# Optimization experiments

Measured on AMD Instinct MI355X. Metric: run time of the kernel, lower is better.

## Reference

```python
import jax, jax.numpy as jnp
import numpy as np

B, S, H = 2, 4096, 1024
NH, BS, NR = 16, 64, 3
HD = H // NH
NB = S // BS
PEN = -10000.0


def setup_inputs():
    key = jax.random.key(0)
    k0, k1, k2, k3 = jax.random.split(key, 4)
    s = 0.02
    inp = {
        'hidden_states': jax.random.normal(k0, (B, S, H), jnp.float32),
        'attention_mask': jnp.ones((B, S), jnp.float32),
        'Wq': jax.random.normal(k1, (H, H), jnp.float32) * s,
        'Wk': jax.random.normal(k2, (H, H), jnp.float32) * s,
        'Wv': jax.random.normal(k3, (H, H), jnp.float32) * s,
        'bq': jnp.zeros((H,), jnp.float32),
        'bk': jnp.zeros((H,), jnp.float32),
        'bv': jnp.zeros((H,), jnp.float32),
    }
    rng = np.random.default_rng(0)
    inp['rand_attn'] = jnp.asarray(rng.integers(1, NB - 1, size=(B, NH, NB - 2, NR)), jnp.int32)
    return inp


def _attend(q_blk, kmat, vmat, mask, rsd):
    # q_blk:[b,h,q,d]  kmat/vmat:[b,h,k,d]  mask: multiplicative {0,1} broadcastable to [b,h,q,k]
    p = jnp.einsum('bhqd,bhkd->bhqk', q_blk, kmat) * rsd + (1.0 - mask) * PEN
    return jnp.einsum('bhqk,bhkd->bhqd', jax.nn.softmax(p, axis=-1), vmat)


def reference(hidden_states, attention_mask, Wq, bq, Wk, bk, Wv, bv, rand_attn):
    b, s, _ = hidden_states.shape
    h, d, bs = NH, HD, BS
    nb = s // bs
    rsd = 1.0 / jnp.sqrt(jnp.asarray(d, hidden_states.dtype))

    def proj(W, bias):
        return (hidden_states @ W + bias).reshape(b, s, h, d).transpose(0, 2, 1, 3)

    q, k, v = proj(Wq, bq), proj(Wk, bk), proj(Wv, bv)  # [b,h,s,d]

    # --- masks (create_masks_for_block_sparse_attn)
    bm = attention_mask.reshape(b, nb, bs)
    band_mask = jnp.einsum('blq,blk->blqk', bm[:, 2:-2],
                           jnp.concatenate([bm[:, 1:-3], bm[:, 2:-2], bm[:, 3:-1]], axis=2))[:, None]
    from_mask = attention_mask.reshape(b, 1, s, 1)
    to_mask = attention_mask.reshape(b, 1, 1, s)

    qb = q.reshape(b, h, nb, bs, d)
    kb = k.reshape(b, h, nb, bs, d)
    vb = v.reshape(b, h, nb, bs, d)

    # --- gather random blocks (jax_gather with batch_dims=2)
    gather2 = jax.vmap(jax.vmap(lambda m, i: m[i]))
    gk = gather2(kb, rand_attn).reshape(b, h, nb - 2, NR * bs, d)
    gv = gather2(vb, rand_attn).reshape(b, h, nb - 2, NR * bs, d)
    rm = jax.vmap(lambda m, i: m[i])(bm, rand_attn).reshape(b, h, nb - 2, NR * bs)
    rand_mask = jnp.einsum('blq,bhlk->bhlqk', bm[:, 1:-1], rm)  # [b,h,nb-2,bs,NR*bs]

    # --- block 0: attends to everything
    first_ctx = _attend(qb[:, :, 0], k, v, to_mask, rsd)[:, :, None]

    # --- block 1: first 3 blocks + last block + its random blocks
    ones_r = jnp.ones((b, 1, 1, NR * bs), q.dtype)
    sk = jnp.concatenate([kb[:, :, 0], kb[:, :, 1], kb[:, :, 2], kb[:, :, -1], gk[:, :, 0]], axis=2)
    sv = jnp.concatenate([vb[:, :, 0], vb[:, :, 1], vb[:, :, 2], vb[:, :, -1], gv[:, :, 0]], axis=2)
    seq_pad = jnp.concatenate([to_mask[:, :, :, :3 * bs], to_mask[:, :, :, -bs:], ones_r], axis=3)
    rand_pad = jnp.concatenate([jnp.ones((b, h, bs, 4 * bs), q.dtype), rand_mask[:, :, 0]], axis=3)
    second_ctx = _attend(qb[:, :, 1], sk, sv, jnp.minimum(seq_pad, rand_pad), rsd)[:, :, None]

    # --- middle blocks 2..nb-3: sliding band + random + first-global + last-global
    mq = qb[:, :, 2:-2]  # [b,h,L,bs,d], L = nb-4
    ek = jnp.concatenate([kb[:, :, 1:-3], kb[:, :, 2:-2], kb[:, :, 3:-1]], axis=3)  # [b,h,L,3bs,d]
    ev = jnp.concatenate([vb[:, :, 1:-3], vb[:, :, 2:-2], vb[:, :, 3:-1]], axis=3)
    band_p = jnp.einsum('bhlqd,bhlkd->bhlqk', mq, ek) * rsd + (1.0 - band_mask) * PEN
    rand_p = jnp.einsum('bhlqd,bhlkd->bhlqk', mq, gk[:, :, 1:-1]) * rsd + (1.0 - rand_mask[:, :, 1:-1]) * PEN
    first_p = jnp.einsum('bhlqd,bhkd->bhlqk', mq, kb[:, :, 0]) * rsd \
        + (1.0 - to_mask[:, :, :, :bs][:, :, :, None]) * PEN
    last_p = jnp.einsum('bhlqd,bhkd->bhlqk', mq, kb[:, :, -1]) * rsd \
        + (1.0 - to_mask[:, :, :, -bs:][:, :, :, None]) * PEN
    # scores layout: [first(bs) | band(3bs) | rand(NR*bs) | last(bs)]
    w = jax.nn.softmax(jnp.concatenate([first_p, band_p, rand_p, last_p], axis=-1), axis=-1)
    mid_ctx = jnp.einsum('bhlqk,bhlkd->bhlqd', w[..., bs:4 * bs], ev)
    mid_ctx += jnp.einsum('bhlqk,bhlkd->bhlqd', w[..., 4 * bs:-bs], gv[:, :, 1:-1])
    mid_ctx += jnp.einsum('bhlqk,bhkd->bhlqd', w[..., :bs], vb[:, :, 0])
    mid_ctx += jnp.einsum('bhlqk,bhkd->bhlqd', w[..., -bs:], vb[:, :, -1])

    # --- block nb-2: first block + last 3 blocks + its random blocks
    slk = jnp.concatenate([kb[:, :, 0], kb[:, :, -3], kb[:, :, -2], kb[:, :, -1], gk[:, :, -1]], axis=2)
    slv = jnp.concatenate([vb[:, :, 0], vb[:, :, -3], vb[:, :, -2], vb[:, :, -1], gv[:, :, -1]], axis=2)
    seq_pad = jnp.concatenate([to_mask[:, :, :, :bs], to_mask[:, :, :, -3 * bs:], ones_r], axis=3)
    rand_pad = jnp.concatenate([jnp.ones((b, h, bs, 4 * bs), q.dtype), rand_mask[:, :, -1]], axis=3)
    seclast_ctx = _attend(qb[:, :, -2], slk, slv, jnp.minimum(seq_pad, rand_pad), rsd)[:, :, None]

    # --- last block: attends to everything
    last_ctx = _attend(qb[:, :, -1], k, v, to_mask, rsd)[:, :, None]

    ctx = jnp.concatenate([first_ctx, second_ctx, mid_ctx, seclast_ctx, last_ctx], axis=2)
    ctx = ctx.reshape(b, h, s, d) * from_mask
    return ctx.transpose(0, 2, 1, 3).reshape(b, s, h * d)
```

## Files before the change

kernel.cpp:

```cpp
#include <hip/hip_runtime.h>

typedef unsigned short u16;
typedef short short8 __attribute__((ext_vector_type(8)));
typedef float f32x4 __attribute__((ext_vector_type(4)));

#define S_TOT 4096
#define NHEAD 16
#define HD 64
#define NB 64
#define BS 64
#define M0 16.0f

__device__ __forceinline__ u16 f2bf(float f) {
    unsigned int u = __builtin_bit_cast(unsigned int, f);
    unsigned int r = (u + 0x7fffu + ((u >> 16) & 1u)) >> 16;
    return (u16)r;
}

__device__ __forceinline__ void gload_lds16(const void* g, void* l) {
    __builtin_amdgcn_global_load_lds(
        (const __attribute__((address_space(1))) unsigned int*)g,
        (__attribute__((address_space(3))) unsigned int*)l, 16, 0, 0);
}

__device__ __forceinline__ float rsum16(float v) {
    v += __shfl_xor(v, 1);
    v += __shfl_xor(v, 2);
    v += __shfl_xor(v, 4);
    v += __shfl_xor(v, 8);
    return v;
}

__global__ __launch_bounds__(256) void convH(const float* __restrict__ h, u16* __restrict__ A) {
    size_t i = (size_t)blockIdx.x * blockDim.x + threadIdx.x;
    float4 v = ((const float4*)h)[i];
    ushort4 o;
    o.x = f2bf(v.x); o.y = f2bf(v.y); o.z = f2bf(v.z); o.w = f2bf(v.w);
    ((ushort4*)A)[i] = o;
}

__global__ __launch_bounds__(256) void transW(const float* __restrict__ Wq,
                                              const float* __restrict__ Wk,
                                              const float* __restrict__ Wv,
                                              u16* __restrict__ Wt) {
    const float* W = blockIdx.z == 0 ? Wq : (blockIdx.z == 1 ? Wk : Wv);
    u16* T = Wt + (size_t)blockIdx.z * 1024 * 1024;
    __shared__ float tile[64][65];
    int n0 = blockIdx.x * 64, k0 = blockIdx.y * 64;
    int tx = threadIdx.x, ty = threadIdx.y;
    for (int r = ty; r < 64; r += 4) tile[r][tx] = W[(size_t)(k0 + r) * 1024 + n0 + tx];
    __syncthreads();
    for (int r = ty; r < 64; r += 4) T[(size_t)(n0 + r) * 1024 + k0 + tx] = f2bf(tile[tx][r]);
}

__global__ __launch_bounds__(256) void gemmQKV(const u16* __restrict__ Ah, const u16* __restrict__ Wt,
                                               const float* __restrict__ bq, const float* __restrict__ bk,
                                               const float* __restrict__ bv,
                                               u16* __restrict__ Qb, u16* __restrict__ Kb,
                                               u16* __restrict__ Vtb) {
    int mode = blockIdx.z;
    const u16* W = Wt + (size_t)mode * 1024 * 1024;
    const float* bias = mode == 0 ? bq : (mode == 1 ? bk : bv);
    __shared__ alignas(16) u16 As[128 * 64];
    __shared__ alignas(16) u16 Bs[128 * 64];
    int tid = threadIdx.x;
    int wave = tid >> 6, lane = tid & 63;
    int lo = lane & 15, hi = lane >> 4;
    int m0 = blockIdx.x * 128, n0 = blockIdx.y * 128;
    int wr = wave >> 1, wc = wave & 1;
    f32x4 acc[4][4];
#pragma unroll
    for (int i = 0; i < 4; i++)
#pragma unroll
        for (int j = 0; j < 4; j++) acc[i][j] = f32x4{0.f, 0.f, 0.f, 0.f};

    for (int k0 = 0; k0 < 1024; k0 += 64) {
#pragma unroll
        for (int i = 0; i < 4; i++) {
            int c = i * 256 + tid;
            int row = c >> 3, c8 = c & 7;
            gload_lds16(Ah + (size_t)(m0 + row) * 1024 + k0 + c8 * 8, As + (i * 256 + wave * 64) * 8);
            gload_lds16(W + (size_t)(n0 + row) * 1024 + k0 + c8 * 8, Bs + (i * 256 + wave * 64) * 8);
        }
        __syncthreads();
#pragma unroll
        for (int kk = 0; kk < 2; kk++) {
            short8 a[4], bb[4];
#pragma unroll
            for (int mi = 0; mi < 4; mi++)
                a[mi] = *(const short8*)&As[(wr * 64 + mi * 16 + lo) * 64 + kk * 32 + hi * 8];
#pragma unroll
            for (int ni = 0; ni < 4; ni++)
                bb[ni] = *(const short8*)&Bs[(wc * 64 + ni * 16 + lo) * 64 + kk * 32 + hi * 8];
#pragma unroll
            for (int mi = 0; mi < 4; mi++)
#pragma unroll
                for (int ni = 0; ni < 4; ni++)
                    acc[mi][ni] = __builtin_amdgcn_mfma_f32_16x16x32_bf16(a[mi], bb[ni], acc[mi][ni], 0, 0, 0);
        }
        __syncthreads();
    }
#pragma unroll
    for (int ni = 0; ni < 4; ni++) {
        int n = n0 + wc * 64 + ni * 16 + lo;
        float bv_ = bias[n];
        int hh = n >> 6, d = n & 63;
        if (mode < 2) {
            u16* T = (mode == 0) ? Qb : Kb;
#pragma unroll
            for (int mi = 0; mi < 4; mi++) {
                int mb = m0 + wr * 64 + mi * 16 + hi * 4;
                int b_ = mb >> 12, s = mb & 4095;
                size_t base = (((size_t)b_ * NHEAD + hh) * S_TOT + s) * HD + d;
#pragma unroll
                for (int r = 0; r < 4; r++) T[base + (size_t)r * HD] = f2bf(acc[mi][ni][r] + bv_);
            }
        } else {
#pragma unroll
            for (int mi = 0; mi < 4; mi++) {
                int mb = m0 + wr * 64 + mi * 16 + hi * 4;
                int b_ = mb >> 12, s = mb & 4095;
                ushort4 pk;
                pk.x = f2bf(acc[mi][ni][0] + bv_);
                pk.y = f2bf(acc[mi][ni][1] + bv_);
                pk.z = f2bf(acc[mi][ni][2] + bv_);
                pk.w = f2bf(acc[mi][ni][3] + bv_);
                *(ushort4*)&Vtb[(((size_t)b_ * NHEAD + hh) * HD + d) * S_TOT + s] = pk;
            }
        }
    }
}

__global__ __launch_bounds__(256) void bigbird_attn(const u16* __restrict__ Qb, const u16* __restrict__ Kb,
                                                    const u16* __restrict__ Vtb, const float* __restrict__ am,
                                                    const int* __restrict__ rand_attn, float* __restrict__ out,
                                                    float* __restrict__ po, float* __restrict__ pl) {
    int lx = blockIdx.x;
    int h = blockIdx.y, b = blockIdx.z;
    bool heavy = lx < 16;
    int p = lx & 7;
    int l = heavy ? ((lx >> 3) ? 63 : 0) : (lx - 15);
    int bh = b * NHEAD + h;
    const u16* Qh = Qb + (size_t)bh * S_TOT * HD;
    const u16* Kh = Kb + (size_t)bh * S_TOT * HD;
    const u16* Vh = Vtb + (size_t)bh * HD * S_TOT;
    int tid = threadIdx.x, wave = tid >> 6, lane = tid & 63;
    int lo = lane & 15, hi = lane >> 4;

    __shared__ int klist[64];
    __shared__ int knum_s;
    __shared__ alignas(16) u16 Kls[2][64 * 64];
    __shared__ alignas(16) u16 Vls[2][64 * 64];
    __shared__ alignas(16) u16 Plds[4][16 * 64];

    auto STAGE = [&](int buf, int kblk) {
        const char* Kc = (const char*)(Kh + (size_t)kblk * BS * HD);
        const char* Vc = (const char*)(Vh + kblk * BS);
#pragma unroll
        for (int i = 0; i < 2; i++) {
            int off = i * 4096 + wave * 1024 + lane * 16;
            int row = off >> 7, c = off & 127;
            int cs = c ^ ((row & 7) << 4);
            gload_lds16(Kc + row * 128 + cs, (char*)Kls[buf] + i * 4096 + wave * 1024);
            gload_lds16(Vc + row * 8192 + cs, (char*)Vls[buf] + i * 4096 + wave * 1024);
        }
    };

    if (tid == 0) {
        if (heavy) {
            for (int i = 0; i < 8; i++) klist[i] = p * 8 + i;
            knum_s = 8;
        } else {
            int q = 0;
            klist[q++] = 0;
            if (l == 1) { klist[q++] = 1; klist[q++] = 2; }
            else if (l == 62) { klist[q++] = 61; klist[q++] = 62; }
            else { klist[q++] = l - 1; klist[q++] = l; klist[q++] = l + 1; }
            klist[q++] = 63;
            const int* ra = rand_attn + (((size_t)b * NHEAD + h) * 62 + (l - 1)) * 3;
            klist[q++] = ra[0]; klist[q++] = ra[1]; klist[q++] = ra[2];
            knum_s = q;
        }
    }
    STAGE(0, heavy ? p * 8 : 0);
    __syncthreads();

    int kn = knum_s;
    int qrow = l * BS + wave * 16;

    short8 qf[2];
#pragma unroll
    for (int kk = 0; kk < 2; kk++)
        qf[kk] = *(const short8*)&Qh[(size_t)(qrow + lo) * HD + kk * 32 + hi * 8];

    float ls[4];
    f32x4 oacc[4];
#pragma unroll
    for (int r = 0; r < 4; r++) ls[r] = 0.f;
#pragma unroll
    for (int n = 0; n < 4; n++) oacc[n] = f32x4{0.f, 0.f, 0.f, 0.f};
    char* pbase = (char*)&Plds[wave][0];

    int buf = 0;
    for (int ci = 0; ci < kn; ci++) {
        int kbase = klist[ci] * BS;
        if (ci + 1 < kn) STAGE(buf ^ 1, klist[ci + 1]);
        float pen[4];
#pragma unroll
        for (int t = 0; t < 4; t++) pen[t] = (1.0f - am[b * S_TOT + kbase + t * 16 + lo]) * (-10000.0f) - M0;
        f32x4 sc[4];
#pragma unroll
        for (int t = 0; t < 4; t++) {
            f32x4 c = f32x4{0.f, 0.f, 0.f, 0.f};
#pragma unroll
            for (int kk = 0; kk < 2; kk++) {
                int kr = t * 16 + lo;
                int a = (kr * 128 + kk * 64 + hi * 16) ^ ((kr & 7) << 4);
                short8 kf = *(const short8*)((char*)Kls[buf] + a);
                c = __builtin_amdgcn_mfma_f32_16x16x32_bf16(qf[kk], kf, c, 0, 0, 0);
            }
            sc[t] = c;
        }
#pragma unroll
        for (int t = 0; t < 4; t++)
#pragma unroll
            for (int r = 0; r < 4; r++) {
                float pr = __expf(sc[t][r] * 0.125f + pen[t]);
                ls[r] += pr;
                int row = hi * 4 + r, col = t * 16 + lo;
                int off = (row * 128 + col * 2) ^ ((row & 7) << 4);
                *(u16*)(pbase + off) = f2bf(pr);
            }
#pragma unroll
        for (int kk = 0; kk < 2; kk++) {
            int off = (lo * 128 + kk * 64 + hi * 16) ^ ((lo & 7) << 4);
            short8 pf = *(const short8*)(pbase + off);
#pragma unroll
            for (int n = 0; n < 4; n++) {
                int vr = n * 16 + lo;
                int a = (vr * 128 + kk * 64 + hi * 16) ^ ((vr & 7) << 4);
                short8 vf = *(const short8*)((char*)Vls[buf] + a);
                oacc[n] = __builtin_amdgcn_mfma_f32_16x16x32_bf16(pf, vf, oacc[n], 0, 0, 0);
            }
        }
        __syncthreads();
        buf ^= 1;
    }

    if (heavy) {
        int combo = (bh << 1) | (l ? 1 : 0);
        int base = (combo * 8 + p) * 64;
#pragma unroll
        for (int r = 0; r < 4; r++) {
            int qr = wave * 16 + hi * 4 + r;
            float lsum = rsum16(ls[r]);
            if (lo == 0) pl[base + qr] = lsum;
#pragma unroll
            for (int n = 0; n < 4; n++)
                po[(size_t)(base + qr) * 64 + n * 16 + lo] = oacc[n][r];
        }
    } else {
#pragma unroll
        for (int r = 0; r < 4; r++) {
            float lsum = rsum16(ls[r]);
            int q = qrow + hi * 4 + r;
            float qm = am[b * S_TOT + q];
            float iv = qm / lsum;
#pragma unroll
            for (int n = 0; n < 4; n++)
                out[((size_t)b * S_TOT + q) * 1024 + h * HD + n * 16 + lo] = oacc[n][r] * iv;
        }
    }
}

__global__ __launch_bounds__(256) void reduce_heavy(const float* __restrict__ po, const float* __restrict__ pl,
                                                    const float* __restrict__ am, float* __restrict__ out) {
    int combo = blockIdx.x;
    int b = combo >> 5, h = (combo >> 1) & 15, hv = combo & 1;
    int l = hv ? 63 : 0;
    for (int idx = threadIdx.x; idx < 4096; idx += 256) {
        int qr = idx >> 6, d = idx & 63;
        float s = 0.f, lsum = 0.f;
#pragma unroll
        for (int p = 0; p < 8; p++) {
            s += po[(size_t)((combo * 8 + p) * 64 + qr) * 64 + d];
            lsum += pl[(combo * 8 + p) * 64 + qr];
        }
        int q = l * BS + qr;
        float qm = am[b * S_TOT + q];
        out[((size_t)b * S_TOT + q) * 1024 + h * HD + d] = s / lsum * qm;
    }
}

extern "C" void kernel_launch(void* const* d_in, const int* in_sizes, int n_in,
                              void* d_out, int out_size, void* d_ws, size_t ws_size,
                              hipStream_t stream) {
    const float* hidden = (const float*)d_in[0];
    const float* am = (const float*)d_in[1];
    const float* Wq = (const float*)d_in[2];
    const float* Wk = (const float*)d_in[3];
    const float* Wv = (const float*)d_in[4];
    const float* bq = (const float*)d_in[5];
    const float* bk = (const float*)d_in[6];
    const float* bv = (const float*)d_in[7];
    const int* rand_attn = (const int*)d_in[8];
    float* out = (float*)d_out;

    char* w = (char*)d_ws;
    u16* Ah = (u16*)w;  w += (size_t)8192 * 1024 * 2;
    u16* Wt = (u16*)w;  w += (size_t)3 * 1024 * 1024 * 2;
    u16* Qb = (u16*)w;  w += (size_t)2 * 16 * 4096 * 64 * 2;
    u16* Kb = (u16*)w;  w += (size_t)2 * 16 * 4096 * 64 * 2;
    u16* Vtb = (u16*)w;
    float* po = (float*)Ah;
    float* pl = po + (size_t)64 * 8 * 64 * 64;

    convH<<<8192, 256, 0, stream>>>(hidden, Ah);
    transW<<<dim3(16, 16, 3), dim3(64, 4), 0, stream>>>(Wq, Wk, Wv, Wt);
    gemmQKV<<<dim3(64, 8, 3), 256, 0, stream>>>(Ah, Wt, bq, bk, bv, Qb, Kb, Vtb);
    bigbird_attn<<<dim3(78, 16, 2), 256, 0, stream>>>(Qb, Kb, Vtb, am, rand_attn, out, po, pl);
    reduce_heavy<<<64, 256, 0, stream>>>(po, pl, am, out);
}
```

Baseline: 165.5 us.

## Double-buffer QKV GEMM with swizzled LDS, block remap, and LDS-staged epilogue

```diff
diff --git a/kernel.cpp b/kernel.cpp
--- a/kernel.cpp
+++ b/kernel.cpp
@@ -53,80 +53,134 @@
     for (int r = ty; r < 64; r += 4) T[(size_t)(n0 + r) * 1024 + k0 + tx] = f2bf(tile[tx][r]);
 }
 
-__global__ __launch_bounds__(256) void gemmQKV(const u16* __restrict__ Ah, const u16* __restrict__ Wt,
-                                               const float* __restrict__ bq, const float* __restrict__ bk,
-                                               const float* __restrict__ bv,
-                                               u16* __restrict__ Qb, u16* __restrict__ Kb,
-                                               u16* __restrict__ Vtb) {
-    int mode = blockIdx.z;
-    const u16* W = Wt + (size_t)mode * 1024 * 1024;
+__global__ __launch_bounds__(256, 2) void gemm_fused(const u16* __restrict__ Ah, const u16* __restrict__ Wt,
+                                                     const float* __restrict__ bq, const float* __restrict__ bk,
+                                                     const float* __restrict__ bv,
+                                                     u16* __restrict__ Qb, u16* __restrict__ Kb,
+                                                     u16* __restrict__ Vtb) {
+    __shared__ alignas(16) char lds[2][32768];
+
+    int bid = blockIdx.x;
+    int swz = (bid & 7) * 192 + (bid >> 3);
+    int bm = swz & 63, bn = swz >> 6;
+    int m0 = bm * 128, n0 = bn * 128;
+    int mode = bn >> 3;
     const float* bias = mode == 0 ? bq : (mode == 1 ? bk : bv);
-    __shared__ alignas(16) u16 As[128 * 64];
-    __shared__ alignas(16) u16 Bs[128 * 64];
-    int tid = threadIdx.x;
-    int wave = tid >> 6, lane = tid & 63;
+    int tid = threadIdx.x, wave = tid >> 6, lane = tid & 63;
     int lo = lane & 15, hi = lane >> 4;
-    int m0 = blockIdx.x * 128, n0 = blockIdx.y * 128;
     int wr = wave >> 1, wc = wave & 1;
+
+    const char* Ac = (const char*)Ah;
+    const char* Wc = (const char*)Wt;
+
+    auto STAGE = [&](int buf, int t) {
+#pragma unroll
+        for (int i = 0; i < 4; i++) {
+            int off = i * 4096 + tid * 16;
+            int row = off >> 7, cb = off & 127;
+            int cs = cb ^ ((row & 7) << 4);
+            char* d = lds[buf] + i * 4096 + wave * 1024;
+            gload_lds16(Ac + (size_t)(m0 + row) * 2048 + t * 128 + cs, d);
+            gload_lds16(Wc + (size_t)(n0 + row) * 2048 + t * 128 + cs, d + 16384);
+        }
+    };
+
     f32x4 acc[4][4];
 #pragma unroll
     for (int i = 0; i < 4; i++)
 #pragma unroll
         for (int j = 0; j < 4; j++) acc[i][j] = f32x4{0.f, 0.f, 0.f, 0.f};
 
-    for (int k0 = 0; k0 < 1024; k0 += 64) {
-#pragma unroll
-        for (int i = 0; i < 4; i++) {
-            int c = i * 256 + tid;
-            int row = c >> 3, c8 = c & 7;
-            gload_lds16(Ah + (size_t)(m0 + row) * 1024 + k0 + c8 * 8, As + (i * 256 + wave * 64) * 8);
-            gload_lds16(W + (size_t)(n0 + row) * 1024 + k0 + c8 * 8, Bs + (i * 256 + wave * 64) * 8);
-        }
+    STAGE(0, 0);
+    asm volatile("s_waitcnt vmcnt(0)" ::: "memory");
+    __builtin_amdgcn_s_barrier();
+    __builtin_amdgcn_sched_barrier(0);
+
+    for (int t = 0; t < 16; t++) {
+        int buf = t & 1;
+        if (t < 15) STAGE(buf ^ 1, t + 1);
+        const char* As = lds[buf];
+        const char* Bs = lds[buf] + 16384;
+        short8 b[4][2];
+#pragma unroll
+        for (int ni = 0; ni < 4; ni++) {
+            int row = wc * 64 + ni * 16 + lo;
+            int sw = (row & 7) << 4;
+#pragma unroll
+            for (int kk = 0; kk < 2; kk++)
+                b[ni][kk] = *(const short8*)(Bs + row * 128 + ((kk * 64 + hi * 16) ^ sw));
+        }
+        __builtin_amdgcn_s_setprio(1);
+#pragma unroll
+        for (int mi = 0; mi < 4; mi++) {
+            int row = wr * 64 + mi * 16 + lo;
+            int sw = (row & 7) << 4;
+            short8 a0 = *(const short8*)(As + row * 128 + ((hi * 16) ^ sw));
+            short8 a1 = *(const short8*)(As + row * 128 + ((64 + hi * 16) ^ sw));
+#pragma unroll
+            for (int ni = 0; ni < 4; ni++) {
+                acc[mi][ni] = __builtin_amdgcn_mfma_f32_16x16x32_bf16(a0, b[ni][0], acc[mi][ni], 0, 0, 0);
+                acc[mi][ni] = __builtin_amdgcn_mfma_f32_16x16x32_bf16(a1, b[ni][1], acc[mi][ni], 0, 0, 0);
+            }
+        }
+        __builtin_amdgcn_s_setprio(0);
+        asm volatile("s_waitcnt vmcnt(0)" ::: "memory");
+        __builtin_amdgcn_s_barrier();
+        __builtin_amdgcn_sched_barrier(0);
+    }
+
+    char* Cs = lds[0];
+    int nb0 = n0 & 1023;
+    float bv4[4];
+#pragma unroll
+    for (int ni = 0; ni < 4; ni++) bv4[ni] = bias[nb0 + wc * 64 + ni * 16 + lo];
+
+    if (mode < 2) {
+#pragma unroll
+        for (int mi = 0; mi < 4; mi++)
+#pragma unroll
+            for (int ni = 0; ni < 4; ni++)
+#pragma unroll
+                for (int r = 0; r < 4; r++) {
+                    int row = wr * 64 + mi * 16 + hi * 4 + r;
+                    int nl = wc * 64 + ni * 16 + lo;
+                    *(u16*)(Cs + ((row * 256 + nl * 2) ^ ((row & 7) << 4))) = f2bf(acc[mi][ni][r] + bv4[ni]);
+                }
         __syncthreads();
-#pragma unroll
-        for (int kk = 0; kk < 2; kk++) {
-            short8 a[4], bb[4];
-#pragma unroll
-            for (int mi = 0; mi < 4; mi++)
-                a[mi] = *(const short8*)&As[(wr * 64 + mi * 16 + lo) * 64 + kk * 32 + hi * 8];
+        u16* T = (mode == 0) ? Qb : Kb;
+#pragma unroll
+        for (int it = 0; it < 8; it++) {
+            int off = it * 4096 + tid * 16;
+            int row = off >> 8, c = off & 255;
+            short8 v = *(const short8*)(Cs + ((row * 256 + c) ^ ((row & 7) << 4)));
+            int nm = nb0 + (c >> 1);
+            int hh = nm >> 6, d = nm & 63;
+            int s = m0 + row;
+            int b_ = s >> 12, sr = s & 4095;
+            *(short8*)&T[(((size_t)b_ * NHEAD + hh) * S_TOT + sr) * HD + d] = v;
+        }
+    } else {
+#pragma unroll
+        for (int mi = 0; mi < 4; mi++)
 #pragma unroll
             for (int ni = 0; ni < 4; ni++)
-                bb[ni] = *(const short8*)&Bs[(wc * 64 + ni * 16 + lo) * 64 + kk * 32 + hi * 8];
-#pragma unroll
-            for (int mi = 0; mi < 4; mi++)
-#pragma unroll
-                for (int ni = 0; ni < 4; ni++)
-                    acc[mi][ni] = __builtin_amdgcn_mfma_f32_16x16x32_bf16(a[mi], bb[ni], acc[mi][ni], 0, 0, 0);
-        }
+#pragma unroll
+                for (int r = 0; r < 4; r++) {
+                    int row = wc * 64 + ni * 16 + lo;
+                    int ml = wr * 64 + mi * 16 + hi * 4 + r;
+                    *(u16*)(Cs + ((row * 256 + ml * 2) ^ ((row & 7) << 4))) = f2bf(acc[mi][ni][r] + bv4[ni]);
+                }
         __syncthreads();
-    }
-#pragma unroll
-    for (int ni = 0; ni < 4; ni++) {
-        int n = n0 + wc * 64 + ni * 16 + lo;
-        float bv_ = bias[n];
-        int hh = n >> 6, d = n & 63;
-        if (mode < 2) {
-            u16* T = (mode == 0) ? Qb : Kb;
-#pragma unroll
-            for (int mi = 0; mi < 4; mi++) {
-                int mb = m0 + wr * 64 + mi * 16 + hi * 4;
-                int b_ = mb >> 12, s = mb & 4095;
-                size_t base = (((size_t)b_ * NHEAD + hh) * S_TOT + s) * HD + d;
-#pragma unroll
-                for (int r = 0; r < 4; r++) T[base + (size_t)r * HD] = f2bf(acc[mi][ni][r] + bv_);
-            }
-        } else {
-#pragma unroll
-            for (int mi = 0; mi < 4; mi++) {
-                int mb = m0 + wr * 64 + mi * 16 + hi * 4;
-                int b_ = mb >> 12, s = mb & 4095;
-                ushort4 pk;
-                pk.x = f2bf(acc[mi][ni][0] + bv_);
-                pk.y = f2bf(acc[mi][ni][1] + bv_);
-                pk.z = f2bf(acc[mi][ni][2] + bv_);
-                pk.w = f2bf(acc[mi][ni][3] + bv_);
-                *(ushort4*)&Vtb[(((size_t)b_ * NHEAD + hh) * HD + d) * S_TOT + s] = pk;
-            }
+#pragma unroll
+        for (int it = 0; it < 8; it++) {
+            int off = it * 4096 + tid * 16;
+            int row = off >> 8, c = off & 255;
+            short8 v = *(const short8*)(Cs + ((row * 256 + c) ^ ((row & 7) << 4)));
+            int dr = nb0 + row;
+            int hh = dr >> 6, d = dr & 63;
+            int s = m0 + (c >> 1);
+            int b_ = s >> 12, sr = s & 4095;
+            *(short8*)&Vtb[(((size_t)b_ * NHEAD + hh) * HD + d) * S_TOT + sr] = v;
         }
     }
 }
@@ -317,7 +371,7 @@
 
     convH<<<8192, 256, 0, stream>>>(hidden, Ah);
     transW<<<dim3(16, 16, 3), dim3(64, 4), 0, stream>>>(Wq, Wk, Wv, Wt);
-    gemmQKV<<<dim3(64, 8, 3), 256, 0, stream>>>(Ah, Wt, bq, bk, bv, Qb, Kb, Vtb);
+    gemm_fused<<<1536, 256, 0, stream>>>(Ah, Wt, bq, bk, bv, Qb, Kb, Vtb);
     bigbird_attn<<<dim3(78, 16, 2), 256, 0, stream>>>(Qb, Kb, Vtb, am, rand_attn, out, po, pl);
     reduce_heavy<<<64, 256, 0, stream>>>(po, pl, am, out);
 }
```

Result: faster. 155.2 us (-6.2%).
